# Performance work log

Hardware: AMD Instinct MI355X
Metric: run time of the kernel (lower is better)

Reference implementation:

```python
import jax, jax.numpy as jnp
import numpy as np

B, T, IN, H, L, CS, OUT = 256, 256, 256, 1024, 8, 10, 64
CHUNK = H // L


def setup_inputs() -> dict:
    key = jax.random.key(0)
    ks = jax.random.split(key, 16)
    G = 4 * H + 2 * L
    s = 0.05
    return {
        "x": jax.random.normal(ks[0], (B, T, IN), jnp.float32),
        "time": jax.random.uniform(ks[1], (B, T, 1), jnp.float32),
        "kernel_w": jax.random.normal(ks[2], (IN + 1, G), jnp.float32) * s,
        "kernel_b": jnp.zeros((G,), jnp.float32),
        "rec_w": jax.random.normal(ks[3], (H + 1, G), jnp.float32) * s,
        "rec_b": jnp.zeros((G,), jnp.float32),
        "scale_w": jax.random.normal(ks[4], (H, H // 6), jnp.float32) * s,
        "scale_b": jnp.zeros((H // 6,), jnp.float32),
        "rescale_w": jax.random.normal(ks[5], (H // 6, H), jnp.float32) * s,
        "rescale_b": jnp.zeros((H,), jnp.float32),
        "conv_w": jax.random.normal(ks[6], (H, H, CS), jnp.float32) * s,  # (out_ch, in_ch, k)
        "conv_b": jnp.zeros((H,), jnp.float32),
        "out_w": jax.random.normal(ks[7], (H, OUT), jnp.float32) * s,
        "out_b": jnp.zeros((OUT,), jnp.float32),
    }


def _stagenet(x, time, kernel_w, kernel_b, rec_w, rec_b, scale_w, scale_b,
              rescale_w, rescale_b, conv_w, conv_b, out_w, out_b):
    batch = x.shape[0]

    def step(carry, xt):
        c, h, tmp_h, tmp_dis = carry
        inp, intv = xt  # (B,IN), (B,1)
        xo = (jnp.concatenate([inp, intv], -1) @ kernel_w + kernel_b
              + jnp.concatenate([h, intv], -1) @ rec_w + rec_b)  # (B, 4H+2L)
        # master gates via cumax
        fm = jnp.cumsum(jax.nn.softmax(xo[:, :L], axis=-1), axis=-1)            # l2r (B,L)
        im_sm = jax.nn.softmax(xo[:, L:2 * L], axis=-1)
        im = jnp.flip(jnp.cumsum(jnp.flip(im_sm, -1), axis=-1), -1)             # r2l (B,L)
        g = xo[:, 2 * L:].reshape(batch, 4 * L, CHUNK)
        f_g = jax.nn.sigmoid(g[:, :L])
        i_g = jax.nn.sigmoid(g[:, L:2 * L])
        o_g = jax.nn.sigmoid(g[:, 2 * L:3 * L])
        c_in = jnp.tanh(g[:, 3 * L:])
        c_l = c.reshape(batch, L, CHUNK)
        fmE, imE = fm[:, :, None], im[:, :, None]
        ov = fmE * imE
        c_new = ov * (f_g * c_l + i_g * c_in) + (fmE - ov) * c_l + (imE - ov) * c_in
        h_new = (o_g * jnp.tanh(c_new)).reshape(batch, H)
        c_new = c_new.reshape(batch, H)
        cur_dis = 1.0 - jnp.mean(fm, -1)                                        # (B,)
        # sliding window buffers
        tmp_h = jnp.concatenate([tmp_h[1:], h_new[None]], 0)                    # (CS,B,H)
        tmp_dis = jnp.concatenate([tmp_dis[1:], cur_dis[None]], 0)              # (CS,B)
        # cumsum-softmax local attention over the window
        ld = jax.nn.softmax(jnp.cumsum(tmp_dis.T, axis=1), axis=1)              # (B,CS)
        lh = tmp_h.transpose(1, 2, 0) * ld[:, None, :]                          # (B,H,CS)
        theme = jnp.mean(lh, -1) @ scale_w + scale_b
        theme = jax.nn.sigmoid(jax.nn.relu(theme) @ rescale_w + rescale_b)      # (B,H)
        conv_out = jnp.einsum('bck,ock->bo', lh, conv_w) + conv_b               # conv1d, out len 1
        local_h = theme * conv_out
        return (c_new, h_new, tmp_h, tmp_dis), (h_new, local_h, cur_dis)

    c0 = jnp.zeros((batch, H), x.dtype)
    h0 = jnp.zeros((batch, H), x.dtype)
    tmp_h0 = jnp.zeros((CS, batch, H), x.dtype)
    tmp_dis0 = jnp.zeros((CS, batch), x.dtype)
    xs = (x.transpose(1, 0, 2), time.transpose(1, 0, 2))
    _, (origin_h, local_h, distance) = jax.lax.scan(step, (c0, h0, tmp_h0, tmp_dis0), xs)
    rnn = (local_h + origin_h).transpose(1, 0, 2)                               # (B,T,H)
    output = jax.nn.sigmoid(rnn @ out_w + out_b)                                # (B,T,OUT)
    return output, distance  # distance: (T,B)


def reference(x, time, kernel_w, kernel_b, rec_w, rec_b, scale_w, scale_b,
              rescale_w, rescale_b, conv_w, conv_b, out_w, out_b):
    return _stagenet(x, time, kernel_w, kernel_b, rec_w, rec_b, scale_w, scale_b,
                     rescale_w, rescale_b, conv_w, conv_b, out_w, out_b)
```

## Files before the change

kernel.cpp:

```cpp
#include <hip/hip_runtime.h>
#include <math.h>

#define BB 256
#define TT 256
#define INW 256
#define HH 1024
#define LL 8
#define CSW 10
#define OUTW 64
#define GG 4112
#define KSEG 1344
#define KTRIP 4032
#define NPAD 4224
#define BH (BB * HH)

typedef __attribute__((ext_vector_type(8))) short short8;
typedef __attribute__((ext_vector_type(4))) float f32x4;

__device__ __forceinline__ float bf2f(ushort u) {
    union { float f; unsigned int i; } v; v.i = ((unsigned int)u) << 16; return v.f;
}
__device__ __forceinline__ ushort f2bf(float f) {
    union { float f; unsigned int i; } v; v.f = f;
    unsigned int r = v.i + 0x7FFFu + ((v.i >> 16) & 1u);
    return (ushort)(r >> 16);
}
__device__ __forceinline__ float sigf(float v) { return 1.0f / (1.0f + expf(-v)); }

template<int WR, int WC, int AMODE, int EPI>
__global__ __launch_bounds__(WR * WC * 64) void mm_kernel(
    const ushort* __restrict__ A, const float* __restrict__ xf,
    const float* __restrict__ tf, const ushort* __restrict__ hR,
    const ushort* __restrict__ hLo,
    const ushort* __restrict__ BT, const float* __restrict__ bias,
    void* __restrict__ Cp, const float* __restrict__ ldw,
    const ushort* __restrict__ TH, float* __restrict__ outp,
    int splitStride, int ldaA, int ldb, int ldc, int K, int t, int RING, int tBase)
{
    constexpr int BM = WR * 64, BN = WC * 64, NT = WR * WC * 64, LS = 72;
    constexpr int AIT = BM * 8 / NT, BIT = BN * 8 / NT;
    __shared__ ushort As[BM * LS];
    __shared__ ushort Bs[BN * LS];
    const int tid = threadIdx.x;
    const int lane = tid & 63, wave = tid >> 6;
    const int wr = wave / WC, wc = wave % WC;

    int bx, by, zSel = 0, kBase = 0;
    if (AMODE == 1) {
        int vid = blockIdx.x;
        int xcd = vid & 7, q = vid >> 3;
        int mem = q & 3, slot = q >> 2;
        int g = slot * 8 + xcd;
        if (g >= 99) return;
        zSel = g / 33; bx = g % 33; by = mem;
        kBase = zSel * KSEG;
    } else {
        bx = blockIdx.x; by = blockIdx.y;
    }
    const int m0 = by * BM, n0 = bx * BN;
    f32x4 acc[4][4] = {};

    auto gather = [&](int ktl, short8* vA, short8* vB) {
#pragma unroll
        for (int i = 0; i < AIT; ++i) {
            int id = tid + i * NT;
            int r = id >> 3, cc = id & 7;
            int k = ktl + cc * 8;
            short8 v;
            if (AMODE == 0) {
                v = *(const short8*)(A + (size_t)(m0 + r) * ldaA + k);
            } else if (AMODE == 1) {
                bool lo = (zSel == 2);
                if (k < 288) {
                    float xv[8];
                    int b = m0 + r;
                    if (k < 256) {
                        const float* src = xf + ((size_t)b * TT + t) * INW + k;
#pragma unroll
                        for (int j = 0; j < 8; ++j) xv[j] = src[j];
                    } else if (k == 256) {
                        float tv = tf[(size_t)b * TT + t];
                        xv[0] = tv; xv[1] = tv;
#pragma unroll
                        for (int j = 2; j < 8; ++j) xv[j] = 0.f;
                    } else {
#pragma unroll
                        for (int j = 0; j < 8; ++j) xv[j] = 0.f;
                    }
                    ushort* po = (ushort*)&v;
#pragma unroll
                    for (int j = 0; j < 8; ++j) {
                        ushort hi = f2bf(xv[j]);
                        po[j] = lo ? f2bf(xv[j] - bf2f(hi)) : hi;
                    }
                } else if (k < 1312) {
                    const ushort* src = lo
                        ? hLo + (size_t)(m0 + r) * HH + (k - 288)
                        : hR + (size_t)((t + 8) % RING) * BH + (size_t)(m0 + r) * HH + (k - 288);
                    v = *(const short8*)src;
                } else {
                    ushort* pz = (ushort*)&v;
#pragma unroll
                    for (int j = 0; j < 8; ++j) pz[j] = 0;
                }
            } else {
                int ks = k >> 10, c = k & 1023;
                int tt = m0 >> 8, b = (m0 & 255) + r;
                int slot = (tBase + tt + ks) % RING;
                short8 hv = *(const short8*)(hR + (size_t)slot * BH + (size_t)b * HH + c);
                float s = ldw[((size_t)tt * 256 + b) * CSW + ks];
                ushort* pv = (ushort*)&hv;
                ushort* po = (ushort*)&v;
#pragma unroll
                for (int j = 0; j < 8; ++j) po[j] = f2bf(bf2f(pv[j]) * s);
            }
            vA[i] = v;
        }
#pragma unroll
        for (int i = 0; i < BIT; ++i) {
            int id = tid + i * NT;
            int n = id >> 3, cc = id & 7;
            vB[i] = *(const short8*)(BT + (size_t)(n0 + n) * ldb + kBase + ktl + cc * 8);
        }
    };

    short8 vA[AIT], vB[BIT];
    gather(0, vA, vB);

    for (int kt = 0; kt < K; kt += 64) {
#pragma unroll
        for (int i = 0; i < AIT; ++i) {
            int id = tid + i * NT;
            *(short8*)(As + (id >> 3) * LS + (id & 7) * 8) = vA[i];
        }
#pragma unroll
        for (int i = 0; i < BIT; ++i) {
            int id = tid + i * NT;
            *(short8*)(Bs + (id >> 3) * LS + (id & 7) * 8) = vB[i];
        }
        __syncthreads();
        if (kt + 64 < K) gather(kt + 64, vA, vB);
#pragma unroll
        for (int kf = 0; kf < 2; ++kf) {
            short8 aF[4], bF[4];
#pragma unroll
            for (int mi = 0; mi < 4; ++mi)
                aF[mi] = *(const short8*)(As + (wr * 64 + mi * 16 + (lane & 15)) * LS + kf * 32 + (lane >> 4) * 8);
#pragma unroll
            for (int ni = 0; ni < 4; ++ni)
                bF[ni] = *(const short8*)(Bs + (wc * 64 + ni * 16 + (lane & 15)) * LS + kf * 32 + (lane >> 4) * 8);
#pragma unroll
            for (int mi = 0; mi < 4; ++mi)
#pragma unroll
                for (int ni = 0; ni < 4; ++ni)
                    acc[mi][ni] = __builtin_amdgcn_mfma_f32_16x16x32_bf16(aF[mi], bF[ni], acc[mi][ni], 0, 0, 0);
        }
        __syncthreads();
    }
#pragma unroll
    for (int mi = 0; mi < 4; ++mi) {
#pragma unroll
        for (int ni = 0; ni < 4; ++ni) {
#pragma unroll
            for (int j = 0; j < 4; ++j) {
                int row = m0 + wr * 64 + mi * 16 + ((lane >> 4) << 2) + j;
                int col = n0 + wc * 64 + ni * 16 + (lane & 15);
                float v = acc[mi][ni][j];
                if (EPI != 0 && bias) v += bias[col];
                if (EPI == 0) {
                    ((float*)Cp)[(size_t)zSel * splitStride + (size_t)row * ldc + col] = v;
                } else if (EPI == 1) {
                    ((ushort*)Cp)[(size_t)row * ldc + col] = f2bf(v > 0.f ? v : 0.f);
                } else if (EPI == 2) {
                    ((ushort*)Cp)[(size_t)row * ldc + col] = f2bf(sigf(v));
                } else if (EPI == 3) {
                    int tt = row >> 8, b = row & 255;
                    int slot = (tBase + tt + 9) % RING;
                    float th = bf2f(TH[(size_t)row * HH + col]);
                    float h  = bf2f(hR[(size_t)slot * BH + (size_t)b * HH + col]);
                    ((ushort*)Cp)[(size_t)row * ldc + col] = f2bf(th * v + h);
                } else {
                    int tt = tBase + (row >> 8), b = row & 255;
                    outp[((size_t)b * TT + tt) * OUTW + col] = sigf(v);
                }
            }
        }
    }
}

__global__ void build_wct(const float* __restrict__ kw, const float* __restrict__ rw,
                          ushort* __restrict__ WcT)
{
    size_t i = (size_t)blockIdx.x * 256 + threadIdx.x;
    if (i >= (size_t)NPAD * KTRIP) return;
    int n = (int)(i / KTRIP), k = (int)(i % KTRIP);
    int sel = k / KSEG, kr = k - sel * KSEG;
    float w = 0.f;
    if (n < GG) {
        if (kr < 256)           w = kw[(size_t)kr * GG + n];
        else if (kr == 256)     w = kw[(size_t)256 * GG + n];
        else if (kr == 257)     w = rw[(size_t)1024 * GG + n];
        else if (kr >= 288 && kr < 1312) w = rw[(size_t)(kr - 288) * GG + n];
    }
    ushort hi = f2bf(w);
    WcT[i] = (sel == 1) ? f2bf(w - bf2f(hi)) : hi;
}

__global__ void build_bc(const float* __restrict__ kb, const float* __restrict__ rb,
                         float* __restrict__ bc)
{
    int i = blockIdx.x * 256 + threadIdx.x;
    if (i < NPAD) bc[i] = (i < GG) ? kb[i] + rb[i] : 0.f;
}

__global__ void build_ctt(const float* __restrict__ cw, ushort* __restrict__ ctT)
{
    size_t i = (size_t)blockIdx.x * 256 + threadIdx.x;
    if (i >= (size_t)HH * HH * CSW) return;
    int o = (int)(i / (HH * CSW)), rest = (int)(i % (HH * CSW));
    int k = rest >> 10, c = rest & 1023;
    ctT[i] = f2bf(cw[((size_t)o * HH + c) * CSW + k]);
}

__global__ void build_swt(const float* __restrict__ sw, const float* __restrict__ sb,
                          ushort* __restrict__ swT, float* __restrict__ sbP)
{
    int i = blockIdx.x * 256 + threadIdx.x;
    if (i < 256 * 1024) {
        int n = i >> 10, k = i & 1023;
        swT[i] = f2bf(n < 170 ? sw[(size_t)k * 170 + n] : 0.f);
    }
    if (i < 256) sbP[i] = (i < 170) ? sb[i] : 0.f;
}

__global__ void build_rswt(const float* __restrict__ rsw, ushort* __restrict__ rswT)
{
    int i = blockIdx.x * 256 + threadIdx.x;
    if (i >= 1024 * 256) return;
    int n = i >> 8, k = i & 255;
    rswT[i] = f2bf(k < 170 ? rsw[(size_t)k * HH + n] : 0.f);
}

__global__ void build_owt(const float* __restrict__ ow, ushort* __restrict__ owT)
{
    int i = blockIdx.x * 256 + threadIdx.x;
    if (i >= OUTW * HH) return;
    int n = i >> 10, k = i & 1023;
    owT[i] = f2bf(ow[(size_t)k * OUTW + n]);
}

__global__ __launch_bounds__(256) void step_kernel(
    const float* __restrict__ xoP, const float* __restrict__ bc,
    float* __restrict__ c, ushort* __restrict__ hR, ushort* __restrict__ hLo,
    float* __restrict__ dist, int t, int RING)
{
    const size_t S = (size_t)BB * NPAD;
    int b = blockIdx.x, tid = threadIdx.x;
    const float* x0 = xoP + (size_t)b * NPAD;
    __shared__ float fm[LL], im[LL];
    if (tid == 0) {
        float xr[2 * LL];
        for (int l = 0; l < 2 * LL; ++l) xr[l] = x0[l] + x0[S + l] + x0[2 * S + l] + bc[l];
        float m1 = -1e30f, m2 = -1e30f;
        for (int l = 0; l < LL; ++l) { m1 = fmaxf(m1, xr[l]); m2 = fmaxf(m2, xr[LL + l]); }
        float e1[LL], e2[LL], s1 = 0.f, s2 = 0.f;
        for (int l = 0; l < LL; ++l) {
            e1[l] = expf(xr[l] - m1); s1 += e1[l];
            e2[l] = expf(xr[LL + l] - m2); s2 += e2[l];
        }
        float cum = 0.f, mean = 0.f;
        for (int l = 0; l < LL; ++l) { cum += e1[l] / s1; fm[l] = cum; mean += cum; }
        float rc = 0.f;
        for (int l = LL - 1; l >= 0; --l) { rc += e2[l] / s2; im[l] = rc; }
        dist[(size_t)t * BB + b] = 1.0f - mean / LL;
    }
    __syncthreads();
    int slot = (t + 9) % RING;
    for (int e = tid; e < HH; e += 256) {
        int l = e >> 7;
        int c0 = 2 * LL + e;
        float f  = sigf(x0[c0] + x0[S + c0] + x0[2 * S + c0] + bc[c0]);
        int c1 = c0 + HH;
        float ig = sigf(x0[c1] + x0[S + c1] + x0[2 * S + c1] + bc[c1]);
        int c2 = c1 + HH;
        float og = sigf(x0[c2] + x0[S + c2] + x0[2 * S + c2] + bc[c2]);
        int c3 = c2 + HH;
        float ci = tanhf(x0[c3] + x0[S + c3] + x0[2 * S + c3] + bc[c3]);
        size_t idx = (size_t)b * HH + e;
        float cl = c[idx];
        float F = fm[l], I = im[l], OV = F * I;
        float cn = OV * (f * cl + ig * ci) + (F - OV) * cl + (I - OV) * ci;
        float hn = og * tanhf(cn);
        c[idx] = cn;
        ushort hi = f2bf(hn);
        hR[(size_t)slot * BH + idx] = hi;
        hLo[idx] = f2bf(hn - bf2f(hi));
    }
}

__global__ void ld_chunk_kernel(const float* __restrict__ dist, float* __restrict__ ldC,
                                int tBase, int Mloc)
{
    int id = blockIdx.x * 256 + threadIdx.x;
    if (id >= Mloc) return;
    int t = tBase + (id >> 8), b = id & 255;
    float cv[CSW], cum = 0.f, mx = -1e30f;
#pragma unroll
    for (int k = 0; k < CSW; ++k) {
        int ts = t - 9 + k;
        cum += (ts >= 0) ? dist[(size_t)ts * BB + b] : 0.f;
        cv[k] = cum; mx = fmaxf(mx, cum);
    }
    float ss = 0.f;
#pragma unroll
    for (int k = 0; k < CSW; ++k) { cv[k] = expf(cv[k] - mx); ss += cv[k]; }
    float inv = 1.0f / ss;
#pragma unroll
    for (int k = 0; k < CSW; ++k) ldC[(size_t)id * CSW + k] = cv[k] * inv;
}

__global__ void mlh_kernel(const ushort* __restrict__ hR, const float* __restrict__ ldC,
                           ushort* __restrict__ MLH, int tBase, int RING)
{
    size_t id = (size_t)blockIdx.x * 256 + threadIdx.x;
    int m = (int)(id >> 7);
    int c0 = ((int)(id & 127)) << 3;
    int t = tBase + (m >> 8), b = m & 255;
    float acc[8] = {};
#pragma unroll
    for (int k = 0; k < CSW; ++k) {
        float s = ldC[(size_t)m * CSW + k];
        int slot = (t + k) % RING;
        short8 hv = *(const short8*)(hR + (size_t)slot * BH + (size_t)b * HH + c0);
        ushort* pv = (ushort*)&hv;
#pragma unroll
        for (int j = 0; j < 8; ++j) acc[j] += bf2f(pv[j]) * s;
    }
#pragma unroll
    for (int j = 0; j < 8; ++j) MLH[(size_t)m * HH + c0 + j] = f2bf(acc[j] * 0.1f);
}

extern "C" void kernel_launch(void* const* d_in, const int* in_sizes, int n_in,
                              void* d_out, int out_size, void* d_ws, size_t ws_size,
                              hipStream_t stream)
{
    const float* x   = (const float*)d_in[0];
    const float* tim = (const float*)d_in[1];
    const float* kw  = (const float*)d_in[2];
    const float* kb  = (const float*)d_in[3];
    const float* rw  = (const float*)d_in[4];
    const float* rb  = (const float*)d_in[5];
    const float* sw  = (const float*)d_in[6];
    const float* sb  = (const float*)d_in[7];
    const float* rsw = (const float*)d_in[8];
    const float* rsb = (const float*)d_in[9];
    const float* cw  = (const float*)d_in[10];
    const float* cb  = (const float*)d_in[11];
    const float* ow  = (const float*)d_in[12];
    const float* ob  = (const float*)d_in[13];
    float* out  = (float*)d_out;
    float* dist = out + (size_t)BB * TT * OUTW;

    auto planSize = [&](int tch) -> size_t {
        size_t o = 0;
        auto al = [&](size_t bytes) { o += (bytes + 255) & ~(size_t)255; };
        int ring = tch + 9;
        al((size_t)ring * BH * 2);
        al((size_t)BH * 2);
        al((size_t)BH * 4);
        al((size_t)NPAD * KTRIP * 2);
        al((size_t)NPAD * 4);
        al((size_t)3 * BB * NPAD * 4);
        al((size_t)tch * 256 * CSW * 4);
        al((size_t)HH * HH * CSW * 2);
        al((size_t)256 * 1024 * 2);
        al((size_t)256 * 4);
        al((size_t)1024 * 256 * 2);
        al((size_t)OUTW * HH * 2);
        al((size_t)tch * 256 * HH * 2);
        al((size_t)tch * 256 * 256 * 2);
        al((size_t)tch * 256 * HH * 2);
        return o;
    };
    const int cands[5] = {64, 32, 16, 8, 4};
    int TCH = 0;
    for (int ci = 0; ci < 5; ++ci)
        if (planSize(cands[ci]) <= ws_size) { TCH = cands[ci]; break; }
    if (TCH == 0) return;
    const int RING = TCH + 9;
    const int Mloc = TCH * 256;

    char* base = (char*)d_ws;
    size_t off = 0;
    auto alloc = [&](size_t bytes) { char* p = base + off; off += (bytes + 255) & ~(size_t)255; return p; };
    ushort* hRing = (ushort*)alloc((size_t)RING * BH * 2);
    ushort* hLo   = (ushort*)alloc((size_t)BH * 2);
    float*  c     = (float*) alloc((size_t)BH * 4);
    ushort* WcT   = (ushort*)alloc((size_t)NPAD * KTRIP * 2);
    float*  bc    = (float*) alloc((size_t)NPAD * 4);
    float*  xoP   = (float*) alloc((size_t)3 * BB * NPAD * 4);
    float*  ldC   = (float*) alloc((size_t)TCH * 256 * CSW * 4);
    ushort* ctT   = (ushort*)alloc((size_t)HH * HH * CSW * 2);
    ushort* swT   = (ushort*)alloc((size_t)256 * 1024 * 2);
    float*  sbP   = (float*) alloc((size_t)256 * 4);
    ushort* rswT  = (ushort*)alloc((size_t)1024 * 256 * 2);
    ushort* owT   = (ushort*)alloc((size_t)OUTW * HH * 2);
    ushort* MLH   = (ushort*)alloc((size_t)TCH * 256 * HH * 2);
    ushort* TH1   = (ushort*)alloc((size_t)TCH * 256 * 256 * 2);
    ushort* TH    = (ushort*)alloc((size_t)TCH * 256 * HH * 2);
    ushort* RNN   = MLH;

    hipMemsetAsync(hRing, 0, (size_t)9 * BH * 2, stream);
    hipMemsetAsync(hLo, 0, (size_t)BH * 2, stream);
    hipMemsetAsync(c, 0, (size_t)BH * 4, stream);

    build_wct<<<(int)(((size_t)NPAD * KTRIP + 255) / 256), 256, 0, stream>>>(kw, rw, WcT);
    build_bc<<<(NPAD + 255) / 256, 256, 0, stream>>>(kb, rb, bc);
    build_ctt<<<(int)(((size_t)HH * HH * CSW + 255) / 256), 256, 0, stream>>>(cw, ctT);
    build_swt<<<(256 * 1024 + 255) / 256, 256, 0, stream>>>(sw, sb, swT, sbP);
    build_rswt<<<(1024 * 256 + 255) / 256, 256, 0, stream>>>(rsw, rswT);
    build_owt<<<(OUTW * HH + 255) / 256, 256, 0, stream>>>(ow, owT);

    const int SPLIT_STRIDE = BB * NPAD;

    for (int tBase = 0; tBase < TT; tBase += TCH) {
        for (int t = tBase; t < tBase + TCH; ++t) {
            mm_kernel<1, 2, 1, 0><<<dim3(416), 128, 0, stream>>>(
                nullptr, x, tim, hRing, hLo, WcT, nullptr, xoP, nullptr, nullptr, nullptr,
                SPLIT_STRIDE, 0, KTRIP, NPAD, KSEG, t, RING, 0);
            step_kernel<<<BB, 256, 0, stream>>>(xoP, bc, c, hRing, hLo, dist, t, RING);
        }
        ld_chunk_kernel<<<Mloc / 256, 256, 0, stream>>>(dist, ldC, tBase, Mloc);
        mlh_kernel<<<Mloc / 2, 256, 0, stream>>>(hRing, ldC, MLH, tBase, RING);
        mm_kernel<2, 2, 0, 1><<<dim3(2, Mloc / 128), 256, 0, stream>>>(
            MLH, nullptr, nullptr, nullptr, nullptr, swT, sbP, TH1, nullptr, nullptr, nullptr,
            0, 1024, 1024, 256, 1024, 0, RING, tBase);
        mm_kernel<2, 2, 0, 2><<<dim3(8, Mloc / 128), 256, 0, stream>>>(
            TH1, nullptr, nullptr, nullptr, nullptr, rswT, rsb, TH, nullptr, nullptr, nullptr,
            0, 256, 256, 1024, 256, 0, RING, tBase);
        mm_kernel<2, 2, 2, 3><<<dim3(8, Mloc / 128), 256, 0, stream>>>(
            nullptr, nullptr, nullptr, hRing, nullptr, ctT, cb, RNN, ldC, TH, nullptr,
            0, 0, HH * CSW, 1024, HH * CSW, 0, RING, tBase);
        mm_kernel<4, 1, 0, 4><<<dim3(1, Mloc / 256), 256, 0, stream>>>(
            RNN, nullptr, nullptr, nullptr, nullptr, owT, ob, nullptr, nullptr, nullptr, out,
            0, 1024, 1024, 0, 1024, 0, RING, tBase);
    }
}
```

Measured before the change: 14.24 ms.

## Split hi/lo recurrent weights and retile per-step GEMM to 128x128 blocks

Splits the combined hi/lo bf16 weight matrix into two separate hi and lo weight arrays. The per-step gate GEMM moves from 64x128 tiles with 128 threads to 128x128 tiles with 256 threads, and work is assigned per XCD panel: the hi-weight panels get four blocks each (hi and lo activation passes) and the lo-weight panels get two. The aim is more reuse of each weight tile per block and fewer redundant activation gathers on this sequential recurrent GEMM. It also swaps the hand-written float-to-bf16 rounding for the library intrinsic, and the larger tiles may lower occupancy.

```diff
diff --git a/kernel.cpp b/kernel.cpp
--- a/kernel.cpp
+++ b/kernel.cpp
@@ -1,4 +1,5 @@
 #include <hip/hip_runtime.h>
+#include <hip/hip_bf16.h>
 #include <math.h>
 
 #define BB 256
@@ -10,9 +11,9 @@
 #define OUTW 64
 #define GG 4112
 #define KSEG 1344
-#define KTRIP 4032
 #define NPAD 4224
 #define BH (BB * HH)
+#define NPANEL 66
 
 typedef __attribute__((ext_vector_type(8))) short short8;
 typedef __attribute__((ext_vector_type(4))) float f32x4;
@@ -21,9 +22,8 @@
     union { float f; unsigned int i; } v; v.i = ((unsigned int)u) << 16; return v.f;
 }
 __device__ __forceinline__ ushort f2bf(float f) {
-    union { float f; unsigned int i; } v; v.f = f;
-    unsigned int r = v.i + 0x7FFFu + ((v.i >> 16) & 1u);
-    return (ushort)(r >> 16);
+    __hip_bfloat16 h = __float2bfloat16(f);
+    return *(ushort*)&h;
 }
 __device__ __forceinline__ float sigf(float v) { return 1.0f / (1.0f + expf(-v)); }
 
@@ -45,15 +45,22 @@
     const int lane = tid & 63, wave = tid >> 6;
     const int wr = wave / WC, wc = wave % WC;
 
-    int bx, by, zSel = 0, kBase = 0;
+    int bx, by, zSel = 0;
+    const ushort* BTeff = BT;
     if (AMODE == 1) {
         int vid = blockIdx.x;
         int xcd = vid & 7, q = vid >> 3;
-        int mem = q & 3, slot = q >> 2;
-        int g = slot * 8 + xcd;
-        if (g >= 99) return;
-        zSel = g / 33; bx = g % 33; by = mem;
-        kBase = zSel * KSEG;
+        int p = -1, mem = 0;
+        for (int j = 0; ; ++j) {
+            int pp = xcd + 8 * j;
+            if (pp >= NPANEL) break;
+            int cc = (pp < 33) ? 4 : 2;
+            if (q < cc) { p = pp; mem = q; break; }
+            q -= cc;
+        }
+        if (p < 0) return;
+        if (p < 33) { bx = p;      zSel = (mem < 2) ? 0 : 2; by = mem & 1; BTeff = BT; }
+        else        { bx = p - 33; zSel = 1;                 by = mem & 1; BTeff = A;  }
     } else {
         bx = blockIdx.x; by = blockIdx.y;
     }
@@ -120,7 +127,7 @@
         for (int i = 0; i < BIT; ++i) {
             int id = tid + i * NT;
             int n = id >> 3, cc = id & 7;
-            vB[i] = *(const short8*)(BT + (size_t)(n0 + n) * ldb + kBase + ktl + cc * 8);
+            vB[i] = *(const short8*)(BTeff + (size_t)(n0 + n) * ldb + ktl + cc * 8);
         }
     };
 
@@ -188,22 +195,22 @@
     }
 }
 
-__global__ void build_wct(const float* __restrict__ kw, const float* __restrict__ rw,
-                          ushort* __restrict__ WcT)
+__global__ void build_whl(const float* __restrict__ kw, const float* __restrict__ rw,
+                          ushort* __restrict__ WhiT, ushort* __restrict__ WloT)
 {
     size_t i = (size_t)blockIdx.x * 256 + threadIdx.x;
-    if (i >= (size_t)NPAD * KTRIP) return;
-    int n = (int)(i / KTRIP), k = (int)(i % KTRIP);
-    int sel = k / KSEG, kr = k - sel * KSEG;
+    if (i >= (size_t)NPAD * KSEG) return;
+    int n = (int)(i / KSEG), k = (int)(i % KSEG);
     float w = 0.f;
     if (n < GG) {
-        if (kr < 256)           w = kw[(size_t)kr * GG + n];
-        else if (kr == 256)     w = kw[(size_t)256 * GG + n];
-        else if (kr == 257)     w = rw[(size_t)1024 * GG + n];
-        else if (kr >= 288 && kr < 1312) w = rw[(size_t)(kr - 288) * GG + n];
+        if (k < 256)           w = kw[(size_t)k * GG + n];
+        else if (k == 256)     w = kw[(size_t)256 * GG + n];
+        else if (k == 257)     w = rw[(size_t)1024 * GG + n];
+        else if (k >= 288 && k < 1312) w = rw[(size_t)(k - 288) * GG + n];
     }
     ushort hi = f2bf(w);
-    WcT[i] = (sel == 1) ? f2bf(w - bf2f(hi)) : hi;
+    WhiT[i] = hi;
+    WloT[i] = f2bf(w - bf2f(hi));
 }
 
 __global__ void build_bc(const float* __restrict__ kb, const float* __restrict__ rb,
@@ -368,7 +375,8 @@
         al((size_t)ring * BH * 2);
         al((size_t)BH * 2);
         al((size_t)BH * 4);
-        al((size_t)NPAD * KTRIP * 2);
+        al((size_t)NPAD * KSEG * 2);
+        al((size_t)NPAD * KSEG * 2);
         al((size_t)NPAD * 4);
         al((size_t)3 * BB * NPAD * 4);
         al((size_t)tch * 256 * CSW * 4);
@@ -396,7 +404,8 @@
     ushort* hRing = (ushort*)alloc((size_t)RING * BH * 2);
     ushort* hLo   = (ushort*)alloc((size_t)BH * 2);
     float*  c     = (float*) alloc((size_t)BH * 4);
-    ushort* WcT   = (ushort*)alloc((size_t)NPAD * KTRIP * 2);
+    ushort* WhiT  = (ushort*)alloc((size_t)NPAD * KSEG * 2);
+    ushort* WloT  = (ushort*)alloc((size_t)NPAD * KSEG * 2);
     float*  bc    = (float*) alloc((size_t)NPAD * 4);
     float*  xoP   = (float*) alloc((size_t)3 * BB * NPAD * 4);
     float*  ldC   = (float*) alloc((size_t)TCH * 256 * CSW * 4);
@@ -414,7 +423,7 @@
     hipMemsetAsync(hLo, 0, (size_t)BH * 2, stream);
     hipMemsetAsync(c, 0, (size_t)BH * 4, stream);
 
-    build_wct<<<(int)(((size_t)NPAD * KTRIP + 255) / 256), 256, 0, stream>>>(kw, rw, WcT);
+    build_whl<<<(int)(((size_t)NPAD * KSEG + 255) / 256), 256, 0, stream>>>(kw, rw, WhiT, WloT);
     build_bc<<<(NPAD + 255) / 256, 256, 0, stream>>>(kb, rb, bc);
     build_ctt<<<(int)(((size_t)HH * HH * CSW + 255) / 256), 256, 0, stream>>>(cw, ctT);
     build_swt<<<(256 * 1024 + 255) / 256, 256, 0, stream>>>(sw, sb, swT, sbP);
@@ -425,9 +434,9 @@
 
     for (int tBase = 0; tBase < TT; tBase += TCH) {
         for (int t = tBase; t < tBase + TCH; ++t) {
-            mm_kernel<1, 2, 1, 0><<<dim3(416), 128, 0, stream>>>(
-                nullptr, x, tim, hRing, hLo, WcT, nullptr, xoP, nullptr, nullptr, nullptr,
-                SPLIT_STRIDE, 0, KTRIP, NPAD, KSEG, t, RING, 0);
+            mm_kernel<2, 2, 1, 0><<<dim3(224), 256, 0, stream>>>(
+                WloT, x, tim, hRing, hLo, WhiT, nullptr, xoP, nullptr, nullptr, nullptr,
+                SPLIT_STRIDE, 0, KSEG, NPAD, KSEG, t, RING, 0);
             step_kernel<<<BB, 256, 0, stream>>>(xoP, bc, c, hRing, hLo, dist, t, RING);
         }
         ld_chunk_kernel<<<Mloc / 256, 256, 0, stream>>>(dist, ldC, tBase, Mloc);
```

Measured after the change: 12.38 ms. -13.1%, faster.
